# Performance work log

Hardware: AMD Instinct MI355X
Metric: run time of the kernel (lower is better)

Reference implementation:

```python
import jax, jax.numpy as jnp
import numpy as np

NUM_BLOCKS = 8
LAMBDA = 0.01  # sparsity_threshold


def softshrink(x, lam):
    return jnp.sign(x) * jnp.maximum(jnp.abs(x) - lam, 0.0)


def setup_inputs() -> dict:
    key = jax.random.key(0)
    ks = jax.random.split(key, 8)
    B, H, W, C = 32, 56, 56, 384
    med = 768
    nb, bs = NUM_BLOCKS, med // NUM_BLOCKS
    scale = 0.02
    return {
        "x": jax.random.normal(ks[0], (B, H, W, C), dtype=jnp.float32),
        "w_pw1": jax.random.normal(ks[1], (C, med), dtype=jnp.float32) * 0.02,
        "star_scale": jnp.ones((1,), dtype=jnp.float32),
        "star_bias": jnp.zeros((1,), dtype=jnp.float32),
        "w1": scale * jax.random.normal(ks[2], (2, nb, bs, bs), dtype=jnp.float32),
        "b1": scale * jax.random.normal(ks[3], (2, nb, bs), dtype=jnp.float32),
        "w2": scale * jax.random.normal(ks[4], (2, nb, bs, bs), dtype=jnp.float32),
        "b2": scale * jax.random.normal(ks[5], (2, nb, bs), dtype=jnp.float32),
        "w_pw2": jax.random.normal(ks[6], (med, C), dtype=jnp.float32) * 0.02,
    }


def reference(x, w_pw1, star_scale, star_bias, w1, b1, w2, b2, w_pw2):
    # pwconv1 (no bias) + StarReLU: s * relu(h)^2 + b
    h = jnp.einsum("bhwc,cm->bhwm", x, w_pw1)
    h = star_scale * jnp.maximum(h, 0.0) ** 2 + star_bias
    h = h.astype(jnp.float32)
    skip = h
    B, H, W, C = h.shape
    nb = NUM_BLOCKS
    bs = C // nb
    Wf = W // 2 + 1

    # 2D real FFT over (H, W), orthonormal
    xf = jnp.fft.rfft2(h, axes=(1, 2), norm="ortho")  # [B,H,Wf,C] complex
    xf = xf.reshape(B, H, Wf, nb, bs)
    xr, xi = jnp.real(xf), jnp.imag(xf)

    # block-diagonal complex MLP, layer 1 (ReLU)
    ein = lambda t, w: jnp.einsum("bhwki,kio->bhwko", t, w)
    o1r = jax.nn.relu(ein(xr, w1[0]) - ein(xi, w1[1]) + b1[0])
    o1i = jax.nn.relu(ein(xi, w1[0]) + ein(xr, w1[1]) + b1[1])

    # layer 2
    o2r = ein(o1r, w2[0]) - ein(o1i, w2[1]) + b2[0]
    o2i = ein(o1i, w2[0]) + ein(o1r, w2[1]) + b2[1]

    # softshrink on real/imag parts, recombine
    o2r = softshrink(o2r, LAMBDA)
    o2i = softshrink(o2i, LAMBDA)
    xc = (o2r + 1j * o2i).reshape(B, H, Wf, C)

    out = jnp.fft.irfft2(xc, s=(H, W), axes=(1, 2), norm="ortho")
    out = out + skip
    # act2 = Identity; pwconv2 (no bias)
    out = jnp.einsum("bhwm,mc->bhwc", out, w_pw2)
    return out
```

## Files before the change

### kernel.cpp

```cpp
#include <hip/hip_runtime.h>
#include <math.h>

#define TWO_PI_F 6.28318530717958647692f

#define MROWS 100352
#define CIN   384
#define MED   768
#define NBLK  8
#define BSZ   96
#define HH    56
#define WWI   56
#define WF    29
#define ROWS2 1792
#define NPOS  51968
#define NROW  2784

#define SZ_XW ((size_t)ROWS2 * WF * BSZ)

#define OFF_CWF 0
#define SZ_CWF  (WF*WWI*2)
#define OFF_HTF (OFF_CWF + SZ_CWF)
#define SZ_HT   (HH*HH*2)
#define OFF_HTI (OFF_HTF + SZ_HT)
#define OFF_IWT (OFF_HTI + SZ_HT)
#define SZ_IWT  (WWI*WF*2)
#define OFF_MID ((size_t)(OFF_IWT + SZ_IWT))
#define SZ_MID  ((size_t)MROWS * MED)
#define OFF_BUF (OFF_MID + SZ_MID)

static __device__ __forceinline__ float softshrink01(float v){
    float t = fabsf(v) - 0.01f;
    return (t > 0.f) ? copysignf(t, v) : 0.f;
}

__global__ __launch_bounds__(256) void init_tables_kernel(
        float* __restrict__ cwF, float* __restrict__ hTf,
        float* __restrict__ hTi, float* __restrict__ iwT)
{
    int tid = threadIdx.x;
    for (int idx = tid; idx < WF * WWI; idx += 256){
        int f = idx / WWI, w = idx % WWI;
        float ang = TWO_PI_F * (float)((f * w) % WWI) / (float)WWI;
        cwF[2*idx]   =  cosf(ang) * (1.f / 56.f);
        cwF[2*idx+1] = -sinf(ang) * (1.f / 56.f);
    }
    for (int idx = tid; idx < HH * HH; idx += 256){
        int k = idx / HH, h = idx % HH;
        float ang = TWO_PI_F * (float)((k * h) % HH) / (float)HH;
        float c = cosf(ang), s = sinf(ang);
        hTf[2*idx]   = c;  hTf[2*idx+1] = -s;
        hTi[2*idx]   = c;  hTi[2*idx+1] =  s;
    }
    for (int idx = tid; idx < WWI * WF; idx += 256){
        int w = idx / WF, f = idx % WF;
        float ang = TWO_PI_F * (float)((f * w) % WWI) / (float)WWI;
        float alpha = (f == 0 || f == WF - 1) ? 1.f : 2.f;
        iwT[2*idx]   =  alpha * cosf(ang) * (1.f / 56.f);
        iwT[2*idx+1] = -alpha * sinf(ang) * (1.f / 56.f);
    }
}

template<bool STAR>
__global__ __launch_bounds__(256) void gemm_kernel(
        const float* __restrict__ A, const float* __restrict__ B,
        float* __restrict__ C, int Kdim, int Ndim,
        const float* __restrict__ sptr, const float* __restrict__ bptr)
{
    __shared__ float As[16][132];
    __shared__ float Bs[16][128];
    const int tid = threadIdx.x;
    const int tx = tid & 15, ty = tid >> 4;
    const int bm = blockIdx.x, bn = blockIdx.y;

    float acc[8][8];
    #pragma unroll
    for (int i = 0; i < 8; ++i)
        #pragma unroll
        for (int j = 0; j < 8; ++j) acc[i][j] = 0.f;

    const float* Aptr = A + (size_t)bm * 128 * Kdim;
    const float* Bptr = B + (size_t)bn * 128;

    for (int k0 = 0; k0 < Kdim; k0 += 16){
        #pragma unroll
        for (int j = 0; j < 2; ++j){
            int m  = (tid >> 2) + j * 64;
            int kc = (tid & 3) * 4;
            const float4 va = *(const float4*)(Aptr + (size_t)m * Kdim + k0 + kc);
            As[kc+0][m] = va.x; As[kc+1][m] = va.y;
            As[kc+2][m] = va.z; As[kc+3][m] = va.w;
        }
        #pragma unroll
        for (int j = 0; j < 2; ++j){
            int kr = (tid >> 5) + j * 8;
            int nc = (tid & 31) * 4;
            *(float4*)(&Bs[kr][nc]) = *(const float4*)(Bptr + (size_t)(k0 + kr) * Ndim + nc);
        }
        __syncthreads();
        #pragma unroll
        for (int k = 0; k < 16; ++k){
            float a[8], b[8];
            *(float4*)(a)   = *(const float4*)(&As[k][ty*4]);
            *(float4*)(a+4) = *(const float4*)(&As[k][64 + ty*4]);
            *(float4*)(b)   = *(const float4*)(&Bs[k][tx*4]);
            *(float4*)(b+4) = *(const float4*)(&Bs[k][64 + tx*4]);
            #pragma unroll
            for (int i = 0; i < 8; ++i)
                #pragma unroll
                for (int j = 0; j < 8; ++j)
                    acc[i][j] = fmaf(a[i], b[j], acc[i][j]);
        }
        __syncthreads();
    }

    float s = 0.f, bb = 0.f;
    if (STAR){ s = sptr[0]; bb = bptr[0]; }
    #pragma unroll
    for (int i = 0; i < 8; ++i){
        int m = bm * 128 + ((i < 4) ? (ty*4 + i) : (64 + ty*4 + (i - 4)));
        #pragma unroll
        for (int jj = 0; jj < 2; ++jj){
            int n = bn * 128 + ((jj == 0) ? (tx*4) : (64 + tx*4));
            float4 v;
            v.x = acc[i][jj*4+0]; v.y = acc[i][jj*4+1];
            v.z = acc[i][jj*4+2]; v.w = acc[i][jj*4+3];
            if (STAR){
                float r;
                r = fmaxf(v.x, 0.f); v.x = fmaf(s*r, r, bb);
                r = fmaxf(v.y, 0.f); v.y = fmaf(s*r, r, bb);
                r = fmaxf(v.z, 0.f); v.z = fmaf(s*r, r, bb);
                r = fmaxf(v.w, 0.f); v.w = fmaf(s*r, r, bb);
            }
            *(float4*)(&C[(size_t)m * Ndim + n]) = v;
        }
    }
}

__global__ __launch_bounds__(256) void fftW_kernel(
        const float* __restrict__ mid, float* __restrict__ AR, float* __restrict__ AI,
        const float* __restrict__ cwF, int blk0)
{
    __shared__ float T[WWI * BSZ];
    const int slot = blockIdx.y;
    const int blk = blk0 + slot;
    const int row2 = blockIdx.x;
    const float* src = mid + (size_t)row2 * WWI * MED + blk * BSZ;
    for (int idx = threadIdx.x; idx < WWI * BSZ; idx += 256){
        int w = idx / BSZ, c = idx - w * BSZ;
        T[idx] = src[(size_t)w * MED + c];
    }
    __syncthreads();
    float* dstR = AR + (size_t)slot * SZ_XW + (size_t)row2 * WF * BSZ;
    float* dstI = AI + (size_t)slot * SZ_XW + (size_t)row2 * WF * BSZ;
    const float2* tw2 = (const float2*)cwF;
    for (int idx = threadIdx.x; idx < WF * BSZ; idx += 256){
        int f = idx / BSZ, c = idx - f * BSZ;
        const float2* tw = tw2 + f * WWI;
        float re = 0.f, im = 0.f;
        #pragma unroll 8
        for (int w = 0; w < WWI; ++w){
            float v = T[w * BSZ + c];
            float2 t = tw[w];
            re = fmaf(v, t.x, re);
            im = fmaf(v, t.y, im);
        }
        dstR[idx] = re;
        dstI[idx] = im;
    }
}

__global__ __launch_bounds__(256) void cgemmH_kernel(
        const float* __restrict__ inR, const float* __restrict__ inI,
        float* __restrict__ outR, float* __restrict__ outI,
        const float* __restrict__ twg)
{
    __shared__ float2 twS[HH * HH];
    __shared__ float2 bS[HH * 48];
    const int slot = blockIdx.y;
    const int b  = blockIdx.x / 58;
    const int n0 = (blockIdx.x - b * 58) * 48;
    const int tid = threadIdx.x;
    const size_t base = (size_t)slot * SZ_XW + (size_t)b * HH * NROW;
    const float* iR = inR + base;
    const float* iI = inI + base;

    const float2* twg2 = (const float2*)twg;
    for (int i = tid; i < HH * HH; i += 256) twS[i] = twg2[i];
    for (int i = tid; i < HH * 48; i += 256){
        int h = i / 48, n = i - h * 48;
        bS[i] = make_float2(iR[(size_t)h * NROW + n0 + n], iI[(size_t)h * NROW + n0 + n]);
    }
    __syncthreads();

    const int ng = tid & 15, kg = tid >> 4;
    if (kg < 14){
        float2 acc[4][3];
        #pragma unroll
        for (int j = 0; j < 4; ++j)
            #pragma unroll
            for (int t = 0; t < 3; ++t) acc[j][t] = make_float2(0.f, 0.f);

        for (int h = 0; h < HH; ++h){
            float2 x0 = bS[h * 48 + ng * 3 + 0];
            float2 x1 = bS[h * 48 + ng * 3 + 1];
            float2 x2 = bS[h * 48 + ng * 3 + 2];
            #pragma unroll
            for (int j = 0; j < 4; ++j){
                float2 w = twS[(kg * 4 + j) * HH + h];
                acc[j][0].x = fmaf(x0.x, w.x, fmaf(-x0.y, w.y, acc[j][0].x));
                acc[j][0].y = fmaf(x0.y, w.x, fmaf( x0.x, w.y, acc[j][0].y));
                acc[j][1].x = fmaf(x1.x, w.x, fmaf(-x1.y, w.y, acc[j][1].x));
                acc[j][1].y = fmaf(x1.y, w.x, fmaf( x1.x, w.y, acc[j][1].y));
                acc[j][2].x = fmaf(x2.x, w.x, fmaf(-x2.y, w.y, acc[j][2].x));
                acc[j][2].y = fmaf(x2.y, w.x, fmaf( x2.x, w.y, acc[j][2].y));
            }
        }
        float* oR = outR + base;
        float* oI = outI + base;
        #pragma unroll
        for (int j = 0; j < 4; ++j){
            int k = kg * 4 + j;
            #pragma unroll
            for (int t = 0; t < 3; ++t){
                int n = n0 + ng * 3 + t;
                oR[(size_t)k * NROW + n] = acc[j][t].x;
                oI[(size_t)k * NROW + n] = acc[j][t].y;
            }
        }
    }
}

template<int ACT>
__global__ __launch_bounds__(256) void cmlp_kernel(
        const float* __restrict__ inR, const float* __restrict__ inI,
        float* __restrict__ outR, float* __restrict__ outI,
        const float* __restrict__ w, const float* __restrict__ bias, int blk0)
{
    __shared__ float2 xS[64 * 24];
    __shared__ float2 wS[24 * 96];
    const int slot = blockIdx.y;
    const int blk = blk0 + slot;
    const int m0 = blockIdx.x * 64;
    const int tid = threadIdx.x;
    const float* W0 = w + (size_t)blk * BSZ * BSZ;
    const float* W1 = w + (size_t)(NBLK + blk) * BSZ * BSZ;
    const size_t base = (size_t)slot * SZ_XW + (size_t)m0 * BSZ;
    const float* iR = inR + base;
    const float* iI = inI + base;
    const int og = tid & 15, mg = tid >> 4;

    float2 acc[4][6];
    #pragma unroll
    for (int j = 0; j < 4; ++j)
        #pragma unroll
        for (int t = 0; t < 6; ++t) acc[j][t] = make_float2(0.f, 0.f);

    for (int i0 = 0; i0 < BSZ; i0 += 24){
        __syncthreads();
        for (int idx = tid; idx < 64 * 24; idx += 256){
            int m = idx / 24, ii = idx - m * 24;
            xS[idx] = make_float2(iR[(size_t)m * BSZ + i0 + ii], iI[(size_t)m * BSZ + i0 + ii]);
        }
        for (int idx = tid; idx < 24 * 96; idx += 256){
            int ii = idx / 96, o = idx - ii * 96;
            wS[idx] = make_float2(W0[(size_t)(i0 + ii) * BSZ + o], W1[(size_t)(i0 + ii) * BSZ + o]);
        }
        __syncthreads();
        for (int ii = 0; ii < 24; ++ii){
            float2 x[4], ww[6];
            #pragma unroll
            for (int j = 0; j < 4; ++j) x[j] = xS[(mg * 4 + j) * 24 + ii];
            #pragma unroll
            for (int t = 0; t < 6; ++t) ww[t] = wS[ii * 96 + og * 6 + t];
            #pragma unroll
            for (int j = 0; j < 4; ++j)
                #pragma unroll
                for (int t = 0; t < 6; ++t){
                    acc[j][t].x = fmaf(x[j].x, ww[t].x, fmaf(-x[j].y, ww[t].y, acc[j][t].x));
                    acc[j][t].y = fmaf(x[j].y, ww[t].x, fmaf( x[j].x, ww[t].y, acc[j][t].y));
                }
        }
    }

    const float* B0 = bias + blk * BSZ;
    const float* B1 = bias + (NBLK + blk) * BSZ;
    float* oR = outR + base;
    float* oI = outI + base;
    #pragma unroll
    for (int t = 0; t < 6; ++t){
        int o = og * 6 + t;
        float br = B0[o], bi = B1[o];
        #pragma unroll
        for (int j = 0; j < 4; ++j){
            float vr = acc[j][t].x + br;
            float vi = acc[j][t].y + bi;
            if (ACT == 1){ vr = fmaxf(vr, 0.f); vi = fmaxf(vi, 0.f); }
            else         { vr = softshrink01(vr); vi = softshrink01(vi); }
            size_t off = (size_t)(mg * 4 + j) * BSZ + o;
            oR[off] = vr;
            oI[off] = vi;
        }
    }
}

__global__ __launch_bounds__(256) void ifftW_kernel(
        const float* __restrict__ AR, const float* __restrict__ AI,
        float* __restrict__ mid, const float* __restrict__ iwT, int blk0)
{
    __shared__ float TR[WF * BSZ];
    __shared__ float TI[WF * BSZ];
    const int slot = blockIdx.y;
    const int blk = blk0 + slot;
    const int row2 = blockIdx.x;
    const float* srcR = AR + (size_t)slot * SZ_XW + (size_t)row2 * WF * BSZ;
    const float* srcI = AI + (size_t)slot * SZ_XW + (size_t)row2 * WF * BSZ;
    for (int idx = threadIdx.x; idx < WF * BSZ; idx += 256){
        TR[idx] = srcR[idx];
        TI[idx] = srcI[idx];
    }
    __syncthreads();
    float* dst = mid + (size_t)row2 * WWI * MED + blk * BSZ;
    const float2* tw2 = (const float2*)iwT;
    for (int idx = threadIdx.x; idx < WWI * BSZ; idx += 256){
        int w = idx / BSZ, c = idx - w * BSZ;
        const float2* t = tw2 + w * WF;
        float acc = 0.f;
        #pragma unroll 8
        for (int fq = 0; fq < WF; ++fq){
            float2 a = t[fq];
            acc = fmaf(TR[fq * BSZ + c], a.x, acc);
            acc = fmaf(TI[fq * BSZ + c], a.y, acc);
        }
        float* p = dst + (size_t)w * MED + c;
        *p = acc + *p;
    }
}

__global__ __launch_bounds__(256) void fusedH_kernel(
        float* __restrict__ XwR, float* __restrict__ XwI,
        const float* __restrict__ w1, const float* __restrict__ b1,
        const float* __restrict__ w2, const float* __restrict__ b2,
        const float* __restrict__ hT, int blk)
{
    extern __shared__ float2 sm2[];
    float2* bufA = sm2;
    float2* bufB = sm2 + 5376;
    float2* wbuf = sm2 + 10752;
    const int tid = threadIdx.x;
    const int b = blockIdx.x / WF, f = blockIdx.x - b * WF;
    float* R = XwR + ((size_t)b * HH * WF + f) * BSZ;
    float* I = XwI + ((size_t)b * HH * WF + f) * BSZ;
    const float2* hTf = (const float2*)hT;
    const int HSTRIDE = WF * BSZ;

    for (int idx = tid; idx < HH * BSZ; idx += 256){
        int h = idx / BSZ, c = idx - h * BSZ;
        bufA[idx] = make_float2(R[(size_t)h * HSTRIDE + c], I[(size_t)h * HSTRIDE + c]);
    }
    __syncthreads();
    for (int idx = tid; idx < HH * BSZ; idx += 256){
        int k = idx / BSZ, c = idx - k * BSZ;
        const float2* tw = hTf + k * HH;
        float re = 0.f, im = 0.f;
        #pragma unroll 8
        for (int h = 0; h < HH; ++h){
            float2 t = bufA[h * BSZ + c];
            float2 w = tw[h];
            re += t.x * w.x + t.y * w.y;
            im += t.y * w.x - t.x * w.y;
        }
        bufB[idx] = make_float2(re, im);
    }
    const float* W10 = w1 + (size_t)blk * BSZ * BSZ;
    const float* W11 = w1 + (size_t)(NBLK + blk) * BSZ * BSZ;
    const float* B10 = b1 + blk * BSZ;
    const float* B11 = b1 + (NBLK + blk) * BSZ;
    #pragma unroll 1
    for (int half = 0; half < 2; ++half){
        const int base = half * 48;
        __syncthreads();
        for (int idx = tid; idx < BSZ * 48; idx += 256){
            int i = idx / 48, oo = idx - i * 48;
            wbuf[idx] = make_float2(W10[i * BSZ + base + oo], W11[i * BSZ + base + oo]);
        }
        __syncthreads();
        for (int t = tid; t < HH * 24; t += 256){
            int row = t / 24, oo = t - row * 24;
            int o = base + oo;
            float2 a0 = make_float2(B10[o],      B11[o]);
            float2 a1 = make_float2(B10[o + 24], B11[o + 24]);
            const float2* xr = bufB + row * BSZ;
            #pragma unroll 8
            for (int i = 0; i < BSZ; ++i){
                float2 x  = xr[i];
                float2 wa = wbuf[i * 48 + oo];
                float2 wb = wbuf[i * 48 + oo + 24];
                a0.x += x.x * wa.x - x.y * wa.y;
                a0.y += x.y * wa.x + x.x * wa.y;
                a1.x += x.x * wb.x - x.y * wb.y;
                a1.y += x.y * wb.x + x.x * wb.y;
            }
            bufA[row * BSZ + o]      = make_float2(fmaxf(a0.x, 0.f), fmaxf(a0.y, 0.f));
            bufA[row * BSZ + o + 24] = make_float2(fmaxf(a1.x, 0.f), fmaxf(a1.y, 0.f));
        }
    }
    const float* W20 = w2 + (size_t)blk * BSZ * BSZ;
    const float* W21 = w2 + (size_t)(NBLK + blk) * BSZ * BSZ;
    const float* B20 = b2 + blk * BSZ;
    const float* B21 = b2 + (NBLK + blk) * BSZ;
    #pragma unroll 1
    for (int half = 0; half < 2; ++half){
        const int base = half * 48;
        __syncthreads();
        for (int idx = tid; idx < BSZ * 48; idx += 256){
            int i = idx / 48, oo = idx - i * 48;
            wbuf[idx] = make_float2(W20[i * BSZ + base + oo], W21[i * BSZ + base + oo]);
        }
        __syncthreads();
        for (int t = tid; t < HH * 24; t += 256){
            int row = t / 24, oo = t - row * 24;
            int o = base + oo;
            float2 a0 = make_float2(B20[o],      B21[o]);
            float2 a1 = make_float2(B20[o + 24], B21[o + 24]);
            const float2* xr = bufA + row * BSZ;
            #pragma unroll 8
            for (int i = 0; i < BSZ; ++i){
                float2 x  = xr[i];
                float2 wa = wbuf[i * 48 + oo];
                float2 wb = wbuf[i * 48 + oo + 24];
                a0.x += x.x * wa.x - x.y * wa.y;
                a0.y += x.y * wa.x + x.x * wa.y;
                a1.x += x.x * wb.x - x.y * wb.y;
                a1.y += x.y * wb.x + x.x * wb.y;
            }
            bufB[row * BSZ + o]      = make_float2(softshrink01(a0.x), softshrink01(a0.y));
            bufB[row * BSZ + o + 24] = make_float2(softshrink01(a1.x), softshrink01(a1.y));
        }
    }
    __syncthreads();
    for (int idx = tid; idx < HH * BSZ; idx += 256){
        int h = idx / BSZ, c = idx - h * BSZ;
        const float2* tw = hTf + h * HH;
        float re = 0.f, im = 0.f;
        #pragma unroll 8
        for (int k = 0; k < HH; ++k){
            float2 t = bufB[k * BSZ + c];
            float2 w = tw[k];
            re += t.x * w.x - t.y * w.y;
            im += t.x * w.y + t.y * w.x;
        }
        R[(size_t)h * HSTRIDE + c] = re;
        I[(size_t)h * HSTRIDE + c] = im;
    }
}

extern "C" void kernel_launch(void* const* d_in, const int* in_sizes, int n_in,
                              void* d_out, int out_size, void* d_ws, size_t ws_size,
                              hipStream_t stream)
{
    (void)in_sizes; (void)n_in; (void)out_size;
    const float* x      = (const float*)d_in[0];
    const float* w_pw1  = (const float*)d_in[1];
    const float* sscale = (const float*)d_in[2];
    const float* sbias  = (const float*)d_in[3];
    const float* w1     = (const float*)d_in[4];
    const float* b1     = (const float*)d_in[5];
    const float* w2     = (const float*)d_in[6];
    const float* b2     = (const float*)d_in[7];
    const float* w_pw2  = (const float*)d_in[8];
    float* out = (float*)d_out;
    float* ws  = (float*)d_ws;

    const size_t bytes_old = (OFF_BUF + 2 * SZ_XW) * sizeof(float);
    const size_t bytes_n1  = (OFF_BUF + 4 * SZ_XW) * sizeof(float);
    const size_t bytes_n8  = (OFF_BUF + 32 * SZ_XW) * sizeof(float);

    int NY;
    bool newpath;
    if      (ws_size >= bytes_n8) { NY = 8; newpath = true; }
    else if (ws_size >= bytes_n1) { NY = 1; newpath = true; }
    else if (ws_size >= bytes_old){ NY = 1; newpath = false; }
    else return;

    float* cwF = ws + OFF_CWF;
    float* hTf = ws + OFF_HTF;
    float* hTi = ws + OFF_HTI;
    float* iwT = ws + OFF_IWT;
    float* mid = ws + OFF_MID;
    float* AR  = ws + OFF_BUF;
    float* AI  = AR + (size_t)NY * SZ_XW;
    float* BR  = AI + (size_t)NY * SZ_XW;
    float* BI  = BR + (size_t)NY * SZ_XW;

    init_tables_kernel<<<1, 256, 0, stream>>>(cwF, hTf, hTi, iwT);

    gemm_kernel<true><<<dim3(MROWS / 128, MED / 128), 256, 0, stream>>>(
        x, w_pw1, mid, CIN, MED, sscale, sbias);

    if (newpath){
        for (int blk0 = 0; blk0 < NBLK; blk0 += NY){
            dim3 gW(ROWS2, NY), gH(32 * 58, NY), gM(NPOS / 64, NY);
            fftW_kernel<<<gW, 256, 0, stream>>>(mid, AR, AI, cwF, blk0);
            cgemmH_kernel<<<gH, 256, 0, stream>>>(AR, AI, BR, BI, hTf);
            cmlp_kernel<1><<<gM, 256, 0, stream>>>(BR, BI, AR, AI, w1, b1, blk0);
            cmlp_kernel<2><<<gM, 256, 0, stream>>>(AR, AI, BR, BI, w2, b2, blk0);
            cgemmH_kernel<<<gH, 256, 0, stream>>>(BR, BI, AR, AI, hTi);
            ifftW_kernel<<<gW, 256, 0, stream>>>(AR, AI, mid, iwT, blk0);
        }
    } else {
        for (int blk = 0; blk < NBLK; ++blk){
            dim3 g1(ROWS2, 1);
            fftW_kernel<<<g1, 256, 0, stream>>>(mid, AR, AI, cwF, blk);
            fusedH_kernel<<<32 * WF, 256, 122880, stream>>>(AR, AI, w1, b1, w2, b2, hTi, blk);
            ifftW_kernel<<<g1, 256, 0, stream>>>(AR, AI, mid, iwT, blk);
        }
    }

    gemm_kernel<false><<<dim3(MROWS / 128, CIN / 128), 256, 0, stream>>>(
        mid, w_pw2, out, MED, CIN, nullptr, nullptr);
}
```

Before: 4.953 ms.

## Use bf16 split-precision MFMA for pointwise GEMMs and block MLP

Replaces the FP32 SIMT pointwise-conv GEMMs with MFMA bf16 GEMMs that use a hi/lo split (three products) to keep near-FP32 accuracy, with pre-pass kernels that convert activations and transpose weights. The complex block-diagonal MLP is recast as a real 192x192 GEMM per block on MFMA, with activations converted to bf16 (single precision only). This adds conversion passes and extra workspace in exchange for matrix-core throughput. The MLP's bf16-only inputs may cost accuracy. The old fused fallback path is removed.

Result: no change. 4.865 ms (-1.8%).

```diff
diff --git a/kernel.cpp b/kernel.cpp
--- a/kernel.cpp
+++ b/kernel.cpp
@@ -16,6 +16,8 @@
 #define NROW  2784
 
 #define SZ_XW ((size_t)ROWS2 * WF * BSZ)
+#define SZ_X  ((size_t)MROWS * CIN)
+#define SZ_MIDE ((size_t)MROWS * MED)
 
 #define OFF_CWF 0
 #define SZ_CWF  (WF*WWI*2)
@@ -25,12 +27,39 @@
 #define OFF_IWT (OFF_HTI + SZ_HT)
 #define SZ_IWT  (WWI*WF*2)
 #define OFF_MID ((size_t)(OFF_IWT + SZ_IWT))
-#define SZ_MID  ((size_t)MROWS * MED)
-#define OFF_BUF (OFF_MID + SZ_MID)
+#define OFF_A   (OFF_MID + SZ_MIDE)
+#define PSLOT8  ((size_t)8 * SZ_XW)
+#define OFF_WMLP(ny) (OFF_A + (size_t)4*(size_t)(ny)*SZ_XW)
+#define SZ_WMLP  (2*8*192*192/2)
+#define SZ_WT1   ((size_t)CIN*MED/2)
 
 static __device__ __forceinline__ float softshrink01(float v){
     float t = fabsf(v) - 0.01f;
     return (t > 0.f) ? copysignf(t, v) : 0.f;
+}
+
+typedef float f32x4 __attribute__((ext_vector_type(4)));
+typedef __bf16 bf16x8v __attribute__((ext_vector_type(8)));
+typedef unsigned short u16x8 __attribute__((ext_vector_type(8)));
+typedef unsigned short u16x4 __attribute__((ext_vector_type(4)));
+
+static __device__ __forceinline__ bf16x8v ld8(const unsigned short* p){
+    return __builtin_bit_cast(bf16x8v, *(const u16x8*)p);
+}
+static __device__ __forceinline__ f32x4 MFMA(bf16x8v a, bf16x8v b, f32x4 c){
+    return __builtin_amdgcn_mfma_f32_16x16x32_bf16(a, b, c, 0, 0, 0);
+}
+static __device__ __forceinline__ unsigned short bfbits(float f){
+    __bf16 h = (__bf16)f;
+    return __builtin_bit_cast(unsigned short, h);
+}
+static __device__ __forceinline__ bf16x8v cvtA8(const float* p){
+    float4 u = *(const float4*)p;
+    float4 v = *(const float4*)(p + 4);
+    bf16x8v r;
+    r[0]=(__bf16)u.x; r[1]=(__bf16)u.y; r[2]=(__bf16)u.z; r[3]=(__bf16)u.w;
+    r[4]=(__bf16)v.x; r[5]=(__bf16)v.y; r[6]=(__bf16)v.z; r[7]=(__bf16)v.w;
+    return r;
 }
 
 __global__ __launch_bounds__(256) void init_tables_kernel(
@@ -60,6 +89,239 @@
     }
 }
 
+__global__ __launch_bounds__(256) void cvt_split_kernel(
+        const float* __restrict__ src, unsigned short* __restrict__ hi,
+        unsigned short* __restrict__ lo, size_t n4)
+{
+    size_t stride = (size_t)gridDim.x * 256;
+    for (size_t i = blockIdx.x * 256 + threadIdx.x; i < n4; i += stride){
+        float4 v = *(const float4*)(src + i * 4);
+        u16x4 h, l;
+        float f, hf;
+        f = v.x; h[0] = bfbits(f); hf = (float)__builtin_bit_cast(__bf16, h[0]); l[0] = bfbits(f - hf);
+        f = v.y; h[1] = bfbits(f); hf = (float)__builtin_bit_cast(__bf16, h[1]); l[1] = bfbits(f - hf);
+        f = v.z; h[2] = bfbits(f); hf = (float)__builtin_bit_cast(__bf16, h[2]); l[2] = bfbits(f - hf);
+        f = v.w; h[3] = bfbits(f); hf = (float)__builtin_bit_cast(__bf16, h[3]); l[3] = bfbits(f - hf);
+        *(u16x4*)(hi + i * 4) = h;
+        *(u16x4*)(lo + i * 4) = l;
+    }
+}
+
+__global__ __launch_bounds__(256) void wT_split_kernel(
+        const float* __restrict__ w, unsigned short* __restrict__ hi,
+        unsigned short* __restrict__ lo, int K, int N)
+{
+    int total = K * N;
+    for (int idx = blockIdx.x * 256 + threadIdx.x; idx < total; idx += gridDim.x * 256){
+        int n = idx / K, k = idx - n * K;
+        float f = w[(size_t)k * N + n];
+        unsigned short h = bfbits(f);
+        float hf = (float)__builtin_bit_cast(__bf16, h);
+        hi[idx] = h;
+        lo[idx] = bfbits(f - hf);
+    }
+}
+
+__global__ __launch_bounds__(256) void wmlp_build_kernel(
+        const float* __restrict__ w1, const float* __restrict__ w2,
+        unsigned short* __restrict__ out)
+{
+    const int total = 2 * 8 * 192 * 192;
+    for (int idx = blockIdx.x * 256 + threadIdx.x; idx < total; idx += gridDim.x * 256){
+        int lay = idx / (8*192*192);
+        int rem = idx - lay * (8*192*192);
+        int blk = rem / (192*192);
+        int rem2 = rem - blk * (192*192);
+        int nn = rem2 / 192, k = rem2 - nn * 192;
+        const float* W = lay ? w2 : w1;
+        bool realn = nn < 96;
+        int o = realn ? nn : nn - 96;
+        float v;
+        if (k < 96){
+            v = realn ? W[((size_t)blk*96 + k)*96 + o]
+                      : W[((size_t)(8+blk)*96 + k)*96 + o];
+        } else {
+            int i = k - 96;
+            v = realn ? -W[((size_t)(8+blk)*96 + i)*96 + o]
+                      :  W[((size_t)blk*96 + i)*96 + o];
+        }
+        out[idx] = bfbits(v);
+    }
+}
+
+#define GSPLIT_MFMA(FH, FL, GH, GL) \
+    _Pragma("unroll") \
+    for (int i = 0; i < 4; ++i){ \
+        _Pragma("unroll") \
+        for (int j = 0; j < 4; ++j){ \
+            acc[i][j] = MFMA(FH[i], GH[j], acc[i][j]); \
+            acc[i][j] = MFMA(FH[i], GL[j], acc[i][j]); \
+            acc[i][j] = MFMA(FL[i], GH[j], acc[i][j]); \
+        } \
+    }
+
+template<bool STAR>
+__global__ __launch_bounds__(256) void gemm_mfma_kernel(
+        const unsigned short* __restrict__ Ah, const unsigned short* __restrict__ Al,
+        const unsigned short* __restrict__ Bh, const unsigned short* __restrict__ Bl,
+        float* __restrict__ C, int Kd, int Nd,
+        const float* __restrict__ sp, const float* __restrict__ bp)
+{
+    const int l = threadIdx.x & 63, wid = threadIdx.x >> 6;
+    const int r = l & 15, g = l >> 4;
+    const int mb = blockIdx.x * 128 + (wid >> 1) * 64;
+    const int nb = blockIdx.y * 128 + (wid & 1) * 64;
+
+    f32x4 acc[4][4];
+    #pragma unroll
+    for (int i = 0; i < 4; ++i)
+        #pragma unroll
+        for (int j = 0; j < 4; ++j)
+            acc[i][j] = (f32x4){0.f, 0.f, 0.f, 0.f};
+
+    size_t aoff[4], boff[4];
+    #pragma unroll
+    for (int i = 0; i < 4; ++i){
+        aoff[i] = (size_t)(mb + i*16 + r) * Kd + 8*g;
+        boff[i] = (size_t)(nb + i*16 + r) * Kd + 8*g;
+    }
+
+    bf16x8v a0h[4], a0l[4], b0h[4], b0l[4];
+    bf16x8v a1h[4], a1l[4], b1h[4], b1l[4];
+    #pragma unroll
+    for (int i = 0; i < 4; ++i){
+        a0h[i] = ld8(Ah + aoff[i]); a0l[i] = ld8(Al + aoff[i]);
+        b0h[i] = ld8(Bh + boff[i]); b0l[i] = ld8(Bl + boff[i]);
+    }
+
+    for (int k0 = 0; k0 < Kd; k0 += 64){
+        #pragma unroll
+        for (int i = 0; i < 4; ++i){
+            a1h[i] = ld8(Ah + aoff[i] + k0 + 32); a1l[i] = ld8(Al + aoff[i] + k0 + 32);
+            b1h[i] = ld8(Bh + boff[i] + k0 + 32); b1l[i] = ld8(Bl + boff[i] + k0 + 32);
+        }
+        GSPLIT_MFMA(a0h, a0l, b0h, b0l)
+        if (k0 + 64 < Kd){
+            #pragma unroll
+            for (int i = 0; i < 4; ++i){
+                a0h[i] = ld8(Ah + aoff[i] + k0 + 64); a0l[i] = ld8(Al + aoff[i] + k0 + 64);
+                b0h[i] = ld8(Bh + boff[i] + k0 + 64); b0l[i] = ld8(Bl + boff[i] + k0 + 64);
+            }
+        }
+        GSPLIT_MFMA(a1h, a1l, b1h, b1l)
+    }
+
+    float s = 0.f, bb = 0.f;
+    if (STAR){ s = sp[0]; bb = bp[0]; }
+    #pragma unroll
+    for (int i = 0; i < 4; ++i){
+        #pragma unroll
+        for (int j = 0; j < 4; ++j){
+            #pragma unroll
+            for (int q = 0; q < 4; ++q){
+                int row = mb + i*16 + 4*g + q;
+                int col = nb + j*16 + r;
+                float v = acc[i][j][q];
+                if (STAR){ float rr = fmaxf(v, 0.f); v = fmaf(s*rr, rr, bb); }
+                C[(size_t)row * Nd + col] = v;
+            }
+        }
+    }
+}
+
+template<int ACT>
+__global__ __launch_bounds__(256) void cmlp_mfma_kernel(
+        const float* __restrict__ inR, const float* __restrict__ inI,
+        float* __restrict__ outR, float* __restrict__ outI,
+        const unsigned short* __restrict__ Wt, const float* __restrict__ bias)
+{
+    const int slot = blockIdx.y;
+    const float* R = inR + (size_t)slot * SZ_XW;
+    const float* I = inI + (size_t)slot * SZ_XW;
+    float* oR = outR + (size_t)slot * SZ_XW;
+    float* oI = outI + (size_t)slot * SZ_XW;
+    const unsigned short* W = Wt + (size_t)slot * 192 * 192;
+
+    const int l = threadIdx.x & 63, wid = threadIdx.x >> 6;
+    const int r = l & 15, g = l >> 4;
+    const int mb = blockIdx.x * 128 + (wid >> 1) * 64;
+    const int nwv = (wid & 1) * 96;
+
+    f32x4 acc[4][6];
+    #pragma unroll
+    for (int i = 0; i < 4; ++i)
+        #pragma unroll
+        for (int j = 0; j < 6; ++j)
+            acc[i][j] = (f32x4){0.f, 0.f, 0.f, 0.f};
+
+    size_t arow[4];
+    #pragma unroll
+    for (int i = 0; i < 4; ++i) arow[i] = (size_t)(mb + i*16 + r) * BSZ;
+    size_t boff[6];
+    #pragma unroll
+    for (int j = 0; j < 6; ++j) boff[j] = (size_t)(nwv + j*16 + r) * 192 + 8*g;
+
+    bf16x8v a0[4], b0[6], a1[4], b1[6];
+    {
+        const float* P = R;
+        #pragma unroll
+        for (int i = 0; i < 4; ++i) a0[i] = cvtA8(P + arow[i] + 8*g);
+        #pragma unroll
+        for (int j = 0; j < 6; ++j) b0[j] = ld8(W + boff[j]);
+    }
+    for (int k0 = 0; k0 < 192; k0 += 64){
+        {
+            int kk = k0 + 32;
+            const float* P = (kk < 96) ? R : I;
+            int c0 = (kk < 96) ? kk : kk - 96;
+            #pragma unroll
+            for (int i = 0; i < 4; ++i) a1[i] = cvtA8(P + arow[i] + c0 + 8*g);
+            #pragma unroll
+            for (int j = 0; j < 6; ++j) b1[j] = ld8(W + boff[j] + kk);
+        }
+        #pragma unroll
+        for (int i = 0; i < 4; ++i)
+            #pragma unroll
+            for (int j = 0; j < 6; ++j)
+                acc[i][j] = MFMA(a0[i], b0[j], acc[i][j]);
+        if (k0 + 64 < 192){
+            int kk = k0 + 64;
+            const float* P = (kk < 96) ? R : I;
+            int c0 = (kk < 96) ? kk : kk - 96;
+            #pragma unroll
+            for (int i = 0; i < 4; ++i) a0[i] = cvtA8(P + arow[i] + c0 + 8*g);
+            #pragma unroll
+            for (int j = 0; j < 6; ++j) b0[j] = ld8(W + boff[j] + kk);
+        }
+        #pragma unroll
+        for (int i = 0; i < 4; ++i)
+            #pragma unroll
+            for (int j = 0; j < 6; ++j)
+                acc[i][j] = MFMA(a1[i], b1[j], acc[i][j]);
+    }
+
+    #pragma unroll
+    for (int j = 0; j < 6; ++j){
+        int col = nwv + j*16 + r;
+        bool realn = col < 96;
+        int o = realn ? col : col - 96;
+        float bv = realn ? bias[(size_t)slot * 96 + o]
+                         : bias[(size_t)(8 + slot) * 96 + o];
+        float* OP = realn ? oR : oI;
+        #pragma unroll
+        for (int i = 0; i < 4; ++i){
+            #pragma unroll
+            for (int q = 0; q < 4; ++q){
+                int row = mb + i*16 + 4*g + q;
+                float v = acc[i][j][q] + bv;
+                if (ACT == 1) v = fmaxf(v, 0.f);
+                else          v = softshrink01(v);
+                OP[(size_t)row * BSZ + o] = v;
+            }
+        }
+    }
+}
+
 template<bool STAR>
 __global__ __launch_bounds__(256) void gemm_kernel(
         const float* __restrict__ A, const float* __restrict__ B,
@@ -125,11 +387,11 @@
             v.x = acc[i][jj*4+0]; v.y = acc[i][jj*4+1];
             v.z = acc[i][jj*4+2]; v.w = acc[i][jj*4+3];
             if (STAR){
-                float r;
-                r = fmaxf(v.x, 0.f); v.x = fmaf(s*r, r, bb);
-                r = fmaxf(v.y, 0.f); v.y = fmaf(s*r, r, bb);
-                r = fmaxf(v.z, 0.f); v.z = fmaf(s*r, r, bb);
-                r = fmaxf(v.w, 0.f); v.w = fmaf(s*r, r, bb);
+                float rr;
+                rr = fmaxf(v.x, 0.f); v.x = fmaf(s*rr, rr, bb);
+                rr = fmaxf(v.y, 0.f); v.y = fmaf(s*rr, rr, bb);
+                rr = fmaxf(v.z, 0.f); v.z = fmaf(s*rr, rr, bb);
+                rr = fmaxf(v.w, 0.f); v.w = fmaf(s*rr, rr, bb);
             }
             *(float4*)(&C[(size_t)m * Ndim + n]) = v;
         }
@@ -336,124 +598,6 @@
     }
 }
 
-__global__ __launch_bounds__(256) void fusedH_kernel(
-        float* __restrict__ XwR, float* __restrict__ XwI,
-        const float* __restrict__ w1, const float* __restrict__ b1,
-        const float* __restrict__ w2, const float* __restrict__ b2,
-        const float* __restrict__ hT, int blk)
-{
-    extern __shared__ float2 sm2[];
-    float2* bufA = sm2;
-    float2* bufB = sm2 + 5376;
-    float2* wbuf = sm2 + 10752;
-    const int tid = threadIdx.x;
-    const int b = blockIdx.x / WF, f = blockIdx.x - b * WF;
-    float* R = XwR + ((size_t)b * HH * WF + f) * BSZ;
-    float* I = XwI + ((size_t)b * HH * WF + f) * BSZ;
-    const float2* hTf = (const float2*)hT;
-    const int HSTRIDE = WF * BSZ;
-
-    for (int idx = tid; idx < HH * BSZ; idx += 256){
-        int h = idx / BSZ, c = idx - h * BSZ;
-        bufA[idx] = make_float2(R[(size_t)h * HSTRIDE + c], I[(size_t)h * HSTRIDE + c]);
-    }
-    __syncthreads();
-    for (int idx = tid; idx < HH * BSZ; idx += 256){
-        int k = idx / BSZ, c = idx - k * BSZ;
-        const float2* tw = hTf + k * HH;
-        float re = 0.f, im = 0.f;
-        #pragma unroll 8
-        for (int h = 0; h < HH; ++h){
-            float2 t = bufA[h * BSZ + c];
-            float2 w = tw[h];
-            re += t.x * w.x + t.y * w.y;
-            im += t.y * w.x - t.x * w.y;
-        }
-        bufB[idx] = make_float2(re, im);
-    }
-    const float* W10 = w1 + (size_t)blk * BSZ * BSZ;
-    const float* W11 = w1 + (size_t)(NBLK + blk) * BSZ * BSZ;
-    const float* B10 = b1 + blk * BSZ;
-    const float* B11 = b1 + (NBLK + blk) * BSZ;
-    #pragma unroll 1
-    for (int half = 0; half < 2; ++half){
-        const int base = half * 48;
-        __syncthreads();
-        for (int idx = tid; idx < BSZ * 48; idx += 256){
-            int i = idx / 48, oo = idx - i * 48;
-            wbuf[idx] = make_float2(W10[i * BSZ + base + oo], W11[i * BSZ + base + oo]);
-        }
-        __syncthreads();
-        for (int t = tid; t < HH * 24; t += 256){
-            int row = t / 24, oo = t - row * 24;
-            int o = base + oo;
-            float2 a0 = make_float2(B10[o],      B11[o]);
-            float2 a1 = make_float2(B10[o + 24], B11[o + 24]);
-            const float2* xr = bufB + row * BSZ;
-            #pragma unroll 8
-            for (int i = 0; i < BSZ; ++i){
-                float2 x  = xr[i];
-                float2 wa = wbuf[i * 48 + oo];
-                float2 wb = wbuf[i * 48 + oo + 24];
-                a0.x += x.x * wa.x - x.y * wa.y;
-                a0.y += x.y * wa.x + x.x * wa.y;
-                a1.x += x.x * wb.x - x.y * wb.y;
-                a1.y += x.y * wb.x + x.x * wb.y;
-            }
-            bufA[row * BSZ + o]      = make_float2(fmaxf(a0.x, 0.f), fmaxf(a0.y, 0.f));
-            bufA[row * BSZ + o + 24] = make_float2(fmaxf(a1.x, 0.f), fmaxf(a1.y, 0.f));
-        }
-    }
-    const float* W20 = w2 + (size_t)blk * BSZ * BSZ;
-    const float* W21 = w2 + (size_t)(NBLK + blk) * BSZ * BSZ;
-    const float* B20 = b2 + blk * BSZ;
-    const float* B21 = b2 + (NBLK + blk) * BSZ;
-    #pragma unroll 1
-    for (int half = 0; half < 2; ++half){
-        const int base = half * 48;
-        __syncthreads();
-        for (int idx = tid; idx < BSZ * 48; idx += 256){
-            int i = idx / 48, oo = idx - i * 48;
-            wbuf[idx] = make_float2(W20[i * BSZ + base + oo], W21[i * BSZ + base + oo]);
-        }
-        __syncthreads();
-        for (int t = tid; t < HH * 24; t += 256){
-            int row = t / 24, oo = t - row * 24;
-            int o = base + oo;
-            float2 a0 = make_float2(B20[o],      B21[o]);
-            float2 a1 = make_float2(B20[o + 24], B21[o + 24]);
-            const float2* xr = bufA + row * BSZ;
-            #pragma unroll 8
-            for (int i = 0; i < BSZ; ++i){
-                float2 x  = xr[i];
-                float2 wa = wbuf[i * 48 + oo];
-                float2 wb = wbuf[i * 48 + oo + 24];
-                a0.x += x.x * wa.x - x.y * wa.y;
-                a0.y += x.y * wa.x + x.x * wa.y;
-                a1.x += x.x * wb.x - x.y * wb.y;
-                a1.y += x.y * wb.x + x.x * wb.y;
-            }
-            bufB[row * BSZ + o]      = make_float2(softshrink01(a0.x), softshrink01(a0.y));
-            bufB[row * BSZ + o + 24] = make_float2(softshrink01(a1.x), softshrink01(a1.y));
-        }
-    }
-    __syncthreads();
-    for (int idx = tid; idx < HH * BSZ; idx += 256){
-        int h = idx / BSZ, c = idx - h * BSZ;
-        const float2* tw = hTf + h * HH;
-        float re = 0.f, im = 0.f;
-        #pragma unroll 8
-        for (int k = 0; k < HH; ++k){
-            float2 t = bufB[k * BSZ + c];
-            float2 w = tw[k];
-            re += t.x * w.x - t.y * w.y;
-            im += t.x * w.y + t.y * w.x;
-        }
-        R[(size_t)h * HSTRIDE + c] = re;
-        I[(size_t)h * HSTRIDE + c] = im;
-    }
-}
-
 extern "C" void kernel_launch(void* const* d_in, const int* in_sizes, int n_in,
                               void* d_out, int out_size, void* d_ws, size_t ws_size,
                               hipStream_t stream)
@@ -471,33 +615,63 @@
     float* out = (float*)d_out;
     float* ws  = (float*)d_ws;
 
-    const size_t bytes_old = (OFF_BUF + 2 * SZ_XW) * sizeof(float);
-    const size_t bytes_n1  = (OFF_BUF + 4 * SZ_XW) * sizeof(float);
-    const size_t bytes_n8  = (OFF_BUF + 32 * SZ_XW) * sizeof(float);
-
-    int NY;
-    bool newpath;
-    if      (ws_size >= bytes_n8) { NY = 8; newpath = true; }
-    else if (ws_size >= bytes_n1) { NY = 1; newpath = true; }
-    else if (ws_size >= bytes_old){ NY = 1; newpath = false; }
-    else return;
+    const size_t fp32_n8_floats = OFF_A + 4 * PSLOT8;
+    const size_t new_floats     = fp32_n8_floats + SZ_WMLP + 4 * SZ_WT1;
+    const size_t bytes_new      = new_floats * sizeof(float);
+    const size_t bytes_f8       = fp32_n8_floats * sizeof(float);
+    const size_t bytes_f1       = (OFF_A + 4 * SZ_XW) * sizeof(float);
 
     float* cwF = ws + OFF_CWF;
     float* hTf = ws + OFF_HTF;
     float* hTi = ws + OFF_HTI;
     float* iwT = ws + OFF_IWT;
     float* mid = ws + OFF_MID;
-    float* AR  = ws + OFF_BUF;
-    float* AI  = AR + (size_t)NY * SZ_XW;
-    float* BR  = AI + (size_t)NY * SZ_XW;
-    float* BI  = BR + (size_t)NY * SZ_XW;
 
     init_tables_kernel<<<1, 256, 0, stream>>>(cwF, hTf, hTi, iwT);
 
-    gemm_kernel<true><<<dim3(MROWS / 128, MED / 128), 256, 0, stream>>>(
-        x, w_pw1, mid, CIN, MED, sscale, sbias);
-
-    if (newpath){
+    if (ws_size >= bytes_new){
+        float* AR = ws + OFF_A;
+        float* AI = AR + PSLOT8;
+        float* BR = AI + PSLOT8;
+        float* BI = BR + PSLOT8;
+        unsigned short* wmlp = (unsigned short*)(ws + fp32_n8_floats);
+        unsigned short* w1Th = (unsigned short*)(ws + fp32_n8_floats + SZ_WMLP);
+        unsigned short* w1Tl = w1Th + (size_t)CIN * MED;
+        unsigned short* w2Th = w1Tl + (size_t)CIN * MED;
+        unsigned short* w2Tl = w2Th + (size_t)CIN * MED;
+        unsigned short* xhi = (unsigned short*)BR;
+        unsigned short* xlo = xhi + SZ_X;
+        unsigned short* mhi = (unsigned short*)BR;
+        unsigned short* mlo = mhi + SZ_MIDE;
+
+        cvt_split_kernel<<<2048, 256, 0, stream>>>(x, xhi, xlo, SZ_X / 4);
+        wT_split_kernel<<<256, 256, 0, stream>>>(w_pw1, w1Th, w1Tl, CIN, MED);
+        wT_split_kernel<<<256, 256, 0, stream>>>(w_pw2, w2Th, w2Tl, MED, CIN);
+        wmlp_build_kernel<<<512, 256, 0, stream>>>(w1, w2, wmlp);
+
+        gemm_mfma_kernel<true><<<dim3(MROWS/128, MED/128), 256, 0, stream>>>(
+            xhi, xlo, w1Th, w1Tl, mid, CIN, MED, sscale, sbias);
+
+        dim3 gW(ROWS2, 8), gH(32 * 58, 8), gM(NPOS / 128, 8);
+        fftW_kernel<<<gW, 256, 0, stream>>>(mid, AR, AI, cwF, 0);
+        cgemmH_kernel<<<gH, 256, 0, stream>>>(AR, AI, BR, BI, hTf);
+        cmlp_mfma_kernel<1><<<gM, 256, 0, stream>>>(BR, BI, AR, AI, wmlp, b1);
+        cmlp_mfma_kernel<2><<<gM, 256, 0, stream>>>(AR, AI, BR, BI, wmlp + (size_t)8*192*192, b2);
+        cgemmH_kernel<<<gH, 256, 0, stream>>>(BR, BI, AR, AI, hTi);
+        ifftW_kernel<<<gW, 256, 0, stream>>>(AR, AI, mid, iwT, 0);
+
+        cvt_split_kernel<<<2048, 256, 0, stream>>>(mid, mhi, mlo, SZ_MIDE / 4);
+        gemm_mfma_kernel<false><<<dim3(MROWS/128, CIN/128), 256, 0, stream>>>(
+            mhi, mlo, w2Th, w2Tl, out, MED, CIN, nullptr, nullptr);
+    } else if (ws_size >= bytes_f8 || ws_size >= bytes_f1){
+        int NY = (ws_size >= bytes_f8) ? 8 : 1;
+        float* AR = ws + OFF_A;
+        float* AI = AR + (size_t)NY * SZ_XW;
+        float* BR = AI + (size_t)NY * SZ_XW;
+        float* BI = BR + (size_t)NY * SZ_XW;
+
+        gemm_kernel<true><<<dim3(MROWS/128, MED/128), 256, 0, stream>>>(
+            x, w_pw1, mid, CIN, MED, sscale, sbias);
         for (int blk0 = 0; blk0 < NBLK; blk0 += NY){
             dim3 gW(ROWS2, NY), gH(32 * 58, NY), gM(NPOS / 64, NY);
             fftW_kernel<<<gW, 256, 0, stream>>>(mid, AR, AI, cwF, blk0);
@@ -507,15 +681,7 @@
             cgemmH_kernel<<<gH, 256, 0, stream>>>(BR, BI, AR, AI, hTi);
             ifftW_kernel<<<gW, 256, 0, stream>>>(AR, AI, mid, iwT, blk0);
         }
-    } else {
-        for (int blk = 0; blk < NBLK; ++blk){
-            dim3 g1(ROWS2, 1);
-            fftW_kernel<<<g1, 256, 0, stream>>>(mid, AR, AI, cwF, blk);
-            fusedH_kernel<<<32 * WF, 256, 122880, stream>>>(AR, AI, w1, b1, w2, b2, hTi, blk);
-            ifftW_kernel<<<g1, 256, 0, stream>>>(AR, AI, mid, iwT, blk);
-        }
-    }
-
-    gemm_kernel<false><<<dim3(MROWS / 128, CIN / 128), 256, 0, stream>>>(
-        mid, w_pw2, out, MED, CIN, nullptr, nullptr);
-}
+        gemm_kernel<false><<<dim3(MROWS/128, CIN/128), 256, 0, stream>>>(
+            mid, w_pw2, out, MED, CIN, nullptr, nullptr);
+    }
+}
```
